# Kernel optimization log

Measured on AMD Instinct MI355X. Metric: run time of the kernel, lower is better.

Reference implementation:

```python
import jax, jax.numpy as jnp
import numpy as np

TOP_K = 4
TAU = 1.0  # training-mode temperature
EPS_NORM = 1e-12
EPS_G = 1e-10


def l2_normalize(x, axis=-1):
    sq = jnp.sum(x * x, axis=axis, keepdims=True)
    return x * jax.lax.rsqrt(jnp.maximum(sq, EPS_NORM))


def setup_inputs() -> dict:
    key = jax.random.key(0)
    k1, k2, k3, k4 = jax.random.split(key, 4)
    B, S, D = 256, 196, 1024
    P, L = 512, 8
    x_embed = jax.random.normal(k1, (B, S, D), dtype=jnp.float32)
    prompt = jax.random.normal(k2, (P, L, D), dtype=jnp.float32) * 0.02
    prompt_key = jax.random.normal(k3, (P, D), dtype=jnp.float32) * 0.02
    gumbel_u = jax.random.uniform(k4, (TOP_K, B, P), dtype=jnp.float32)
    return {"x_embed": x_embed, "prompt": prompt, "prompt_key": prompt_key,
            "gumbel_u": gumbel_u}


def reference(x_embed, prompt, prompt_key, gumbel_u):
    # query: mean over sequence dim (embedding_key='mean')  -> [B, D]
    query = jnp.mean(x_embed, axis=1)
    key_n = l2_normalize(prompt_key, axis=1)   # [P, D]
    q_n = l2_normalize(query, axis=1)          # [B, D]
    sim = jnp.matmul(q_n, key_n.T)             # [B, P]

    P = prompt.shape[0]
    cur = sim
    selected = []
    for i in range(TOP_K):
        # Gumbel(0,1) noise from uniform samples
        g = -jnp.log(-jnp.log(gumbel_u[i] + EPS_G) + EPS_G)
        soft = jax.nn.softmax((cur + g) / TAU, axis=-1)      # [B, P]
        hard = jax.nn.one_hot(jnp.argmax(soft, axis=-1), P, dtype=soft.dtype)
        w = soft + jax.lax.stop_gradient(hard - soft)        # straight-through
        # weighted combination over pool -> [B, L, D]
        sel = jnp.einsum('bp,pld->bld', w, prompt)
        selected.append(sel)
        # training-mode mask-out of selected entries
        cur = cur - w * 1000.0
    return jnp.concatenate(selected, axis=1)  # [B, TOP_K*L, D]
```

## Files before the change

kernel.cpp:

```cpp
#include <hip/hip_runtime.h>
#include <math.h>

#define B    256
#define S    196
#define D    1024
#define P    512
#define L    8
#define TOPK 4

#define KSPLIT 8
#define RPG 49
#define PKB 32
#define PK_PER_BLOCK 16

__global__ __launch_bounds__(1024) void query_norm_kernel(
    const float* __restrict__ x, const float* __restrict__ pk,
    float* __restrict__ qm, float* __restrict__ alpha,
    float* __restrict__ beta) {
  const int t = threadIdx.x;
  const int lane = t & 63;
  const int w = t >> 6;

  if (blockIdx.x >= B) {
    const int p = (blockIdx.x - B) * PK_PER_BLOCK + w;
    const float* kp = pk + (size_t)p * D;
    float ss = 0.f;
#pragma unroll
    for (int j = 0; j < 4; ++j) {
      float4 v = *(const float4*)(kp + lane * 4 + j * 256);
      ss += v.x * v.x + v.y * v.y + v.z * v.z + v.w * v.w;
    }
    for (int off = 32; off > 0; off >>= 1) ss += __shfl_down(ss, off, 64);
    if (lane == 0) beta[p] = rsqrtf(fmaxf(ss, 1e-12f));
    return;
  }

  const int b = blockIdx.x;
  const int g = t >> 8;
  const int c = t & 255;
  const float* xb =
      x + (size_t)b * S * D + (size_t)g * RPG * D + c * 4;

  float4 acc = make_float4(0.f, 0.f, 0.f, 0.f);
#pragma unroll 7
  for (int s = 0; s < RPG; ++s) {
    float4 v = *(const float4*)(xb + (size_t)s * D);
    acc.x += v.x; acc.y += v.y; acc.z += v.z; acc.w += v.w;
  }

  __shared__ float4 red[3][256];
  __shared__ float wsum[4];
  if (g > 0) red[g - 1][c] = acc;
  __syncthreads();

  if (g == 0) {
    float4 r0 = red[0][c], r1 = red[1][c], r2 = red[2][c];
    acc.x += r0.x + r1.x + r2.x;
    acc.y += r0.y + r1.y + r2.y;
    acc.z += r0.z + r1.z + r2.z;
    acc.w += r0.w + r1.w + r2.w;
    const float inv = 1.0f / (float)S;
    acc.x *= inv; acc.y *= inv; acc.z *= inv; acc.w *= inv;
    *(float4*)(qm + (size_t)b * D + c * 4) = acc;
    float ss = acc.x * acc.x + acc.y * acc.y + acc.z * acc.z + acc.w * acc.w;
    for (int off = 32; off > 0; off >>= 1) ss += __shfl_down(ss, off, 64);
    if (lane == 0) wsum[w] = ss;
  }
  __syncthreads();
  if (t == 0)
    alpha[b] = rsqrtf(fmaxf(wsum[0] + wsum[1] + wsum[2] + wsum[3], 1e-12f));
}

#define KK 16
__global__ __launch_bounds__(256) void sim_kernel(
    const float* __restrict__ qm, const float* __restrict__ pk,
    float* __restrict__ simp) {
  const int b0 = blockIdx.x * 64;
  const int p0 = blockIdx.y * 64;
  const int z  = blockIdx.z;
  const int k0 = z * (D / KSPLIT);
  const int t = threadIdx.x;
  const int tx = t & 15;
  const int ty = t >> 4;

  __shared__ float As[KK][68];
  __shared__ float Bs[KK][68];

  float acc[4][4];
#pragma unroll
  for (int i = 0; i < 4; ++i)
#pragma unroll
    for (int j = 0; j < 4; ++j) acc[i][j] = 0.f;

  const int rr = t >> 2;
  const int k4 = (t & 3) * 4;

  for (int kt = 0; kt < D / KSPLIT; kt += KK) {
    float4 a = *(const float4*)(qm + (size_t)(b0 + rr) * D + k0 + kt + k4);
    float4 bb = *(const float4*)(pk + (size_t)(p0 + rr) * D + k0 + kt + k4);
    As[k4 + 0][rr] = a.x; As[k4 + 1][rr] = a.y;
    As[k4 + 2][rr] = a.z; As[k4 + 3][rr] = a.w;
    Bs[k4 + 0][rr] = bb.x; Bs[k4 + 1][rr] = bb.y;
    Bs[k4 + 2][rr] = bb.z; Bs[k4 + 3][rr] = bb.w;
    __syncthreads();
#pragma unroll
    for (int kk = 0; kk < KK; ++kk) {
      float4 av = *(const float4*)&As[kk][ty * 4];
      float4 bv = *(const float4*)&Bs[kk][tx * 4];
      acc[0][0] += av.x * bv.x; acc[0][1] += av.x * bv.y;
      acc[0][2] += av.x * bv.z; acc[0][3] += av.x * bv.w;
      acc[1][0] += av.y * bv.x; acc[1][1] += av.y * bv.y;
      acc[1][2] += av.y * bv.z; acc[1][3] += av.y * bv.w;
      acc[2][0] += av.z * bv.x; acc[2][1] += av.z * bv.y;
      acc[2][2] += av.z * bv.z; acc[2][3] += av.z * bv.w;
      acc[3][0] += av.w * bv.x; acc[3][1] += av.w * bv.y;
      acc[3][2] += av.w * bv.z; acc[3][3] += av.w * bv.w;
    }
    __syncthreads();
  }
#pragma unroll
  for (int i = 0; i < 4; ++i)
#pragma unroll
    for (int j = 0; j < 4; ++j)
      simp[((size_t)z * B + b0 + ty * 4 + i) * P + p0 + tx * 4 + j] =
          acc[i][j];
}

__global__ __launch_bounds__(512) void select_kernel(
    const float* __restrict__ simp, const float* __restrict__ alpha,
    const float* __restrict__ beta, const float* __restrict__ gu,
    int* __restrict__ sidx) {
  const int b = blockIdx.x;
  const int t = threadIdx.x;
  const int lane = t & 63, wv = t >> 6;

  float c = 0.f;
#pragma unroll
  for (int z = 0; z < KSPLIT; ++z)
    c += simp[((size_t)z * B + b) * P + t];
  c *= alpha[b] * beta[t];

  float g[TOPK];
#pragma unroll
  for (int i = 0; i < TOPK; ++i) {
    float u = gu[((size_t)i * B + b) * P + t];
    g[i] = -logf(-logf(u + 1e-10f) + 1e-10f);
  }

  __shared__ float wval[8];
  __shared__ int   widx[8];
  __shared__ int   ssel[TOPK];

  for (int i = 0; i < TOPK; ++i) {
    float v = c + g[i];
    int idx = t;
    for (int off = 32; off > 0; off >>= 1) {
      float ov = __shfl_down(v, off, 64);
      int oi = __shfl_down(idx, off, 64);
      if (ov > v || (ov == v && oi < idx)) { v = ov; idx = oi; }
    }
    if (lane == 0) { wval[wv] = v; widx[wv] = idx; }
    __syncthreads();
    if (t == 0) {
      float bv = wval[0]; int bi = widx[0];
#pragma unroll
      for (int k = 1; k < 8; ++k)
        if (wval[k] > bv || (wval[k] == bv && widx[k] < bi)) {
          bv = wval[k]; bi = widx[k];
        }
      ssel[i] = bi;
    }
    __syncthreads();
    if (t == ssel[i]) c -= 1000.0f;
  }
  if (t < TOPK) sidx[b * TOPK + t] = ssel[t];
}

__global__ __launch_bounds__(256) void gather_kernel(
    const int* __restrict__ sidx, const float* __restrict__ prompt,
    float* __restrict__ out) {
  const int bi = blockIdx.x;
  const int h = blockIdx.y;
  const int t = threadIdx.x;
  const int p = sidx[bi];
  const float4* src =
      (const float4*)(prompt + (size_t)p * L * D) + h * 1024;
  float4* dst = (float4*)(out + (size_t)bi * (L * D)) + h * 1024;
#pragma unroll
  for (int c = 0; c < 4; ++c)
    dst[c * 256 + t] = src[c * 256 + t];
}

extern "C" void kernel_launch(void* const* d_in, const int* in_sizes, int n_in,
                              void* d_out, int out_size, void* d_ws,
                              size_t ws_size, hipStream_t stream) {
  const float* x_embed    = (const float*)d_in[0];
  const float* prompt     = (const float*)d_in[1];
  const float* prompt_key = (const float*)d_in[2];
  const float* gumbel_u   = (const float*)d_in[3];
  float* out = (float*)d_out;

  float* simp  = (float*)d_ws;
  float* qm    = simp + (size_t)KSPLIT * B * P;
  float* alpha = qm + (size_t)B * D;
  float* beta  = alpha + B;
  int*   sidx  = (int*)(beta + P);

  query_norm_kernel<<<B + PKB, 1024, 0, stream>>>(x_embed, prompt_key, qm,
                                                  alpha, beta);
  sim_kernel<<<dim3(B / 64, P / 64, KSPLIT), 256, 0, stream>>>(qm, prompt_key,
                                                               simp);
  select_kernel<<<B, 512, 0, stream>>>(simp, alpha, beta, gumbel_u, sidx);
  gather_kernel<<<dim3(B * TOPK, 2), 256, 0, stream>>>(sidx, prompt, out);
}
```

Measured before the change: 327.2 us.

## Fuse all stages into one cooperative kernel with grid syncs

Replaces the four launches (mean/normalize, similarity GEMM, Gumbel top-k select, gather) with a single cooperative kernel of 256 blocks of 1024 threads, separated by grid.sync. The aim is to remove launch gaps and inter-kernel round trips. In exchange the GEMM phase now uses 1024 threads per block with 2x2 register tiles instead of 4x4. Each block then does both the selection and the gather for its own batch row. If the cooperative launch fails, it falls back to the original four-kernel path.

```diff
diff --git a/kernel.cpp b/kernel.cpp
--- a/kernel.cpp
+++ b/kernel.cpp
@@ -1,5 +1,8 @@
 #include <hip/hip_runtime.h>
+#include <hip/hip_cooperative_groups.h>
 #include <math.h>
+
+namespace cg = cooperative_groups;
 
 #define B    256
 #define S    196
@@ -10,8 +13,149 @@
 
 #define KSPLIT 8
 #define RPG 49
+#define KK 16
 #define PKB 32
 #define PK_PER_BLOCK 16
+
+__global__ __launch_bounds__(1024, 4) void fused_all_kernel(
+    const float* __restrict__ x, const float* __restrict__ pk,
+    const float* __restrict__ gu, const float* __restrict__ prompt,
+    float* __restrict__ out, float* __restrict__ simp,
+    float* __restrict__ qm, float* __restrict__ beta) {
+  cg::grid_group grid = cg::this_grid();
+  const int blk = blockIdx.x;
+  const int t = threadIdx.x;
+  const int lane = t & 63;
+  const int w = t >> 6;
+
+  __shared__ float4 red[3][256];
+  __shared__ float wsum[4];
+  __shared__ float s_alpha;
+  __shared__ float As[KK][65];
+  __shared__ float Bs[KK][65];
+  __shared__ float wval[8];
+  __shared__ int   widx[8];
+  __shared__ int   ssel[TOPK];
+
+  {
+    const int g = t >> 8;
+    const int c = t & 255;
+    const float* xb = x + (size_t)blk * S * D + (size_t)g * RPG * D + c * 4;
+    float4 acc = make_float4(0.f, 0.f, 0.f, 0.f);
+#pragma unroll 7
+    for (int s = 0; s < RPG; ++s) {
+      float4 v = *(const float4*)(xb + (size_t)s * D);
+      acc.x += v.x; acc.y += v.y; acc.z += v.z; acc.w += v.w;
+    }
+    if (g > 0) red[g - 1][c] = acc;
+    __syncthreads();
+    if (g == 0) {
+      float4 r0 = red[0][c], r1 = red[1][c], r2 = red[2][c];
+      acc.x += r0.x + r1.x + r2.x;
+      acc.y += r0.y + r1.y + r2.y;
+      acc.z += r0.z + r1.z + r2.z;
+      acc.w += r0.w + r1.w + r2.w;
+      const float inv = 1.0f / (float)S;
+      acc.x *= inv; acc.y *= inv; acc.z *= inv; acc.w *= inv;
+      *(float4*)(qm + (size_t)blk * D + c * 4) = acc;
+      float ss =
+          acc.x * acc.x + acc.y * acc.y + acc.z * acc.z + acc.w * acc.w;
+      for (int off = 32; off > 0; off >>= 1) ss += __shfl_down(ss, off, 64);
+      if (lane == 0) wsum[w] = ss;
+    } else if (w == 12 || w == 13) {
+      const int p = blk * 2 + (w - 12);
+      const float* kp = pk + (size_t)p * D;
+      float ss = 0.f;
+#pragma unroll
+      for (int j = 0; j < 4; ++j) {
+        float4 v = *(const float4*)(kp + lane * 4 + j * 256);
+        ss += v.x * v.x + v.y * v.y + v.z * v.z + v.w * v.w;
+      }
+      for (int off = 32; off > 0; off >>= 1) ss += __shfl_down(ss, off, 64);
+      if (lane == 0) beta[p] = rsqrtf(fmaxf(ss, 1e-12f));
+    }
+    __syncthreads();
+    if (t == 0)
+      s_alpha =
+          rsqrtf(fmaxf(wsum[0] + wsum[1] + wsum[2] + wsum[3], 1e-12f));
+  }
+  grid.sync();
+
+  {
+    const int bz = blk >> 5;
+    const int by = (blk >> 2) & 7;
+    const int bx = blk & 3;
+    const int b0 = bx * 64, p0 = by * 64, k0 = bz * (D / KSPLIT);
+    const int lr = t >> 4;
+    const int lk = t & 15;
+    const int tx = t & 31;
+    const int ty = t >> 5;
+    float a00 = 0.f, a01 = 0.f, a10 = 0.f, a11 = 0.f;
+    for (int kt = 0; kt < D / KSPLIT; kt += KK) {
+      As[lk][lr] = qm[(size_t)(b0 + lr) * D + k0 + kt + lk];
+      Bs[lk][lr] = pk[(size_t)(p0 + lr) * D + k0 + kt + lk];
+      __syncthreads();
+#pragma unroll
+      for (int kk = 0; kk < KK; ++kk) {
+        float av0 = As[kk][ty * 2], av1 = As[kk][ty * 2 + 1];
+        float bv0 = Bs[kk][tx * 2], bv1 = Bs[kk][tx * 2 + 1];
+        a00 += av0 * bv0; a01 += av0 * bv1;
+        a10 += av1 * bv0; a11 += av1 * bv1;
+      }
+      __syncthreads();
+    }
+    float* sp = simp + ((size_t)bz * B + b0 + ty * 2) * P + p0 + tx * 2;
+    sp[0] = a00; sp[1] = a01; sp[P] = a10; sp[P + 1] = a11;
+  }
+  grid.sync();
+
+  float cval = 0.f;
+  float gn[TOPK];
+  if (t < P) {
+#pragma unroll
+    for (int z = 0; z < KSPLIT; ++z)
+      cval += simp[((size_t)z * B + blk) * P + t];
+    cval *= s_alpha * beta[t];
+#pragma unroll
+    for (int i = 0; i < TOPK; ++i) {
+      float u = gu[((size_t)i * B + blk) * P + t];
+      gn[i] = -logf(-logf(u + 1e-10f) + 1e-10f);
+    }
+  }
+  for (int i = 0; i < TOPK; ++i) {
+    if (t < P) {
+      float v = cval + gn[i];
+      int idx = t;
+      for (int off = 32; off > 0; off >>= 1) {
+        float ov = __shfl_down(v, off, 64);
+        int oi = __shfl_down(idx, off, 64);
+        if (ov > v || (ov == v && oi < idx)) { v = ov; idx = oi; }
+      }
+      if (lane == 0) { wval[w] = v; widx[w] = idx; }
+    }
+    __syncthreads();
+    if (t == 0) {
+      float bv = wval[0]; int bi = widx[0];
+#pragma unroll
+      for (int k2 = 1; k2 < 8; ++k2)
+        if (wval[k2] > bv || (wval[k2] == bv && widx[k2] < bi)) {
+          bv = wval[k2]; bi = widx[k2];
+        }
+      ssel[i] = bi;
+    }
+    __syncthreads();
+    if (t < P && t == ssel[i]) cval -= 1000.f;
+  }
+
+#pragma unroll
+  for (int i = 0; i < TOPK; ++i) {
+    const int p = ssel[i];
+    const float4* src = (const float4*)(prompt + (size_t)p * L * D);
+    float4* dst = (float4*)(out + ((size_t)blk * (TOPK * L) + i * L) * D);
+    dst[t] = src[t];
+    dst[t + 1024] = src[t + 1024];
+  }
+}
 
 __global__ __launch_bounds__(1024) void query_norm_kernel(
     const float* __restrict__ x, const float* __restrict__ pk,
@@ -38,8 +182,7 @@
   const int b = blockIdx.x;
   const int g = t >> 8;
   const int c = t & 255;
-  const float* xb =
-      x + (size_t)b * S * D + (size_t)g * RPG * D + c * 4;
+  const float* xb = x + (size_t)b * S * D + (size_t)g * RPG * D + c * 4;
 
   float4 acc = make_float4(0.f, 0.f, 0.f, 0.f);
 #pragma unroll 7
@@ -71,7 +214,6 @@
     alpha[b] = rsqrtf(fmaxf(wsum[0] + wsum[1] + wsum[2] + wsum[3], 1e-12f));
 }
 
-#define KK 16
 __global__ __launch_bounds__(256) void sim_kernel(
     const float* __restrict__ qm, const float* __restrict__ pk,
     float* __restrict__ simp) {
@@ -83,8 +225,8 @@
   const int tx = t & 15;
   const int ty = t >> 4;
 
-  __shared__ float As[KK][68];
-  __shared__ float Bs[KK][68];
+  __shared__ float As2[KK][68];
+  __shared__ float Bs2[KK][68];
 
   float acc[4][4];
 #pragma unroll
@@ -98,15 +240,15 @@
   for (int kt = 0; kt < D / KSPLIT; kt += KK) {
     float4 a = *(const float4*)(qm + (size_t)(b0 + rr) * D + k0 + kt + k4);
     float4 bb = *(const float4*)(pk + (size_t)(p0 + rr) * D + k0 + kt + k4);
-    As[k4 + 0][rr] = a.x; As[k4 + 1][rr] = a.y;
-    As[k4 + 2][rr] = a.z; As[k4 + 3][rr] = a.w;
-    Bs[k4 + 0][rr] = bb.x; Bs[k4 + 1][rr] = bb.y;
-    Bs[k4 + 2][rr] = bb.z; Bs[k4 + 3][rr] = bb.w;
+    As2[k4 + 0][rr] = a.x; As2[k4 + 1][rr] = a.y;
+    As2[k4 + 2][rr] = a.z; As2[k4 + 3][rr] = a.w;
+    Bs2[k4 + 0][rr] = bb.x; Bs2[k4 + 1][rr] = bb.y;
+    Bs2[k4 + 2][rr] = bb.z; Bs2[k4 + 3][rr] = bb.w;
     __syncthreads();
 #pragma unroll
     for (int kk = 0; kk < KK; ++kk) {
-      float4 av = *(const float4*)&As[kk][ty * 4];
-      float4 bv = *(const float4*)&Bs[kk][tx * 4];
+      float4 av = *(const float4*)&As2[kk][ty * 4];
+      float4 bv = *(const float4*)&Bs2[kk][tx * 4];
       acc[0][0] += av.x * bv.x; acc[0][1] += av.x * bv.y;
       acc[0][2] += av.x * bv.z; acc[0][3] += av.x * bv.w;
       acc[1][0] += av.y * bv.x; acc[1][1] += av.y * bv.y;
@@ -206,10 +348,17 @@
   float* beta  = alpha + B;
   int*   sidx  = (int*)(beta + P);
 
-  query_norm_kernel<<<B + PKB, 1024, 0, stream>>>(x_embed, prompt_key, qm,
-                                                  alpha, beta);
-  sim_kernel<<<dim3(B / 64, P / 64, KSPLIT), 256, 0, stream>>>(qm, prompt_key,
-                                                               simp);
-  select_kernel<<<B, 512, 0, stream>>>(simp, alpha, beta, gumbel_u, sidx);
-  gather_kernel<<<dim3(B * TOPK, 2), 256, 0, stream>>>(sidx, prompt, out);
-}
+  void* args[] = {(void*)&x_embed, (void*)&prompt_key, (void*)&gumbel_u,
+                  (void*)&prompt,  (void*)&out,        (void*)&simp,
+                  (void*)&qm,      (void*)&beta};
+  hipError_t err = hipLaunchCooperativeKernel(
+      (const void*)fused_all_kernel, dim3(B), dim3(1024), args, 0, stream);
+  if (err != hipSuccess) {
+    query_norm_kernel<<<B + PKB, 1024, 0, stream>>>(x_embed, prompt_key, qm,
+                                                    alpha, beta);
+    sim_kernel<<<dim3(B / 64, P / 64, KSPLIT), 256, 0, stream>>>(
+        qm, prompt_key, simp);
+    select_kernel<<<B, 512, 0, stream>>>(simp, alpha, beta, gumbel_u, sidx);
+    gather_kernel<<<dim3(B * TOPK, 2), 256, 0, stream>>>(sidx, prompt, out);
+  }
+}
```

Measured after the change: 395.5 us. +20.9%, slower.
